# Performance work log

Hardware: AMD Instinct MI355X
Metric: run time of the kernel (lower is better)

## Reference

```python
import jax, jax.numpy as jnp
import numpy as np

B, S, D = 4, 2048, 512
H, DK = 16, 32  # n_heads, d_k == d_v == args.mid_dim


def setup_inputs() -> dict:
    key = jax.random.key(0)
    ks = jax.random.split(key, 9)
    s = 0.02
    return {
        "x": jax.random.normal(ks[0], (B, S, D), dtype=jnp.float32),
        "Wq": jax.random.normal(ks[1], (D, H * DK), dtype=jnp.float32) * s,
        "bq": jnp.zeros((H * DK,), dtype=jnp.float32),
        "Wk": jax.random.normal(ks[2], (D, H * DK), dtype=jnp.float32) * s,
        "bk": jnp.zeros((H * DK,), dtype=jnp.float32),
        "Wv": jax.random.normal(ks[3], (D, H * DK), dtype=jnp.float32) * s,
        "bv": jnp.zeros((H * DK,), dtype=jnp.float32),
        "Wo": jax.random.normal(ks[4], (H * DK, D), dtype=jnp.float32) * s,
        "bo": jnp.zeros((D,), dtype=jnp.float32),
        "mask_border": 64,
    }


def reference(x, Wq, bq, Wk, bk, Wv, bv, Wo, bo, mask_border):
    b, s, d = x.shape
    # band mask: tril(ones, border) * triu(ones, -border) == 1 where |i-j| <= border
    i = jnp.arange(s)
    band = (jnp.abs(i[:, None] - i[None, :]) <= mask_border).astype(x.dtype)  # [S,S]

    q = (x @ Wq + bq).reshape(b, s, H, DK)
    k = (x @ Wk + bk).reshape(b, s, H, DK)
    v = (x @ Wv + bv).reshape(b, s, H, DK)

    scale = 1.0 / jnp.sqrt(jnp.asarray(DK, x.dtype))
    # float attn_mask is ADDED to scores (PatchTST-style _ScaledDotProductAttention)
    scores = jnp.einsum("bihd,bjhd->bhij", q, k) * scale + band[None, None]
    attn = jax.nn.softmax(scores, axis=-1)
    o = jnp.einsum("bhij,bjhd->bihd", attn, v).reshape(b, s, H * DK)
    out_1 = o @ Wo + bo  # [B,S,D]

    # reconstruction score + quantiles (side stats; do not feed returned tensor)
    rec_score = jnp.mean((out_1 - x) ** 2, axis=2)  # [B,S]
    q1, q2, q3 = jnp.quantile(rec_score, jnp.array([0.25, 0.5, 0.75], rec_score.dtype), axis=-1)
    del q1, q2, q3

    # tmp = out_1 - x; out_1 = x + tmp  (identity); module returns out_1
    return out_1
```

## Files before the change

### kernel.cpp

```cpp
#include <hip/hip_runtime.h>
#include <hip/hip_bf16.h>

#define B_ 4
#define S_ 2048
#define D_ 512
#define H_ 16
#define DK_ 32
#define MS_ 8192

typedef unsigned short u16;
typedef __attribute__((ext_vector_type(4))) unsigned short u16x4;
typedef __attribute__((ext_vector_type(8))) short bf16x8;
typedef __attribute__((ext_vector_type(4))) float f32x4;

union pbu { unsigned u[4]; bf16x8 v; };

__device__ __forceinline__ u16 f2b(float f) {
    union { float f; unsigned u; } uf; uf.f = f;
    unsigned u = uf.u;
    unsigned r = u + 0x7fffu + ((u >> 16) & 1u);
    return (u16)(r >> 16);
}

__device__ __forceinline__ unsigned cvt_pk_bf16(float lo, float hi) {
    unsigned r;
    asm("v_cvt_pk_bf16_f32 %0, %1, %2" : "=v"(r) : "v"(lo), "v"(hi));
    return r;
}

__device__ __forceinline__ void gload16(const u16* src, u16* dst) {
    __builtin_amdgcn_global_load_lds(
        (const __attribute__((address_space(1))) unsigned int*)src,
        (__attribute__((address_space(3))) unsigned int*)dst, 16, 0, 0);
}

__global__ void cast_f32_to_bf16(const float* __restrict__ in, u16* __restrict__ out, int n4) {
    int i = blockIdx.x * blockDim.x + threadIdx.x;
    if (i >= n4) return;
    f32x4 v = *(const f32x4*)(in + (size_t)i * 4);
    u16x4 o;
    o[0] = f2b(v[0]); o[1] = f2b(v[1]); o[2] = f2b(v[2]); o[3] = f2b(v[3]);
    *(u16x4*)(out + (size_t)i * 4) = o;
}

__global__ void transpose_cast(const float* __restrict__ Wq, const float* __restrict__ Wk,
                               const float* __restrict__ Wv, const float* __restrict__ Wo,
                               u16* __restrict__ out) {
    const int z = blockIdx.z;
    const float* W = (z == 0) ? Wq : (z == 1) ? Wk : (z == 2) ? Wv : Wo;
    u16* O = out + (size_t)z * D_ * D_;
    __shared__ float T[32][33];
    const int n0 = blockIdx.x * 32, k0 = blockIdx.y * 32;
    const int tx = threadIdx.x & 31, ty = threadIdx.x >> 5;
#pragma unroll
    for (int i = 0; i < 4; i++) {
        int row = ty + 8 * i;
        T[tx][row] = W[(size_t)(k0 + row) * D_ + n0 + tx];
    }
    __syncthreads();
#pragma unroll
    for (int i = 0; i < 4; i++) {
        int row = ty + 8 * i;
        O[(size_t)(n0 + row) * D_ + k0 + tx] = f2b(T[row][tx]);
    }
}

__launch_bounds__(256)
__global__ void gemm_qkv(const u16* __restrict__ Xb, const u16* __restrict__ WT,
                         const float* __restrict__ bq, const float* __restrict__ bk, const float* __restrict__ bv,
                         u16* __restrict__ Qw, u16* __restrict__ Kw, u16* __restrict__ Vw) {
    const int which = blockIdx.z;
    const u16* Wt = WT + (size_t)which * D_ * D_;
    const float* bias = (which == 0) ? bq : (which == 1) ? bk : bv;
    u16* Out = (which == 0) ? Qw : (which == 1) ? Kw : Vw;
    const float oscale = (which == 0) ? (float)(1.4426950408889634 / 5.656854249492381) : 1.0f;

    __shared__ __attribute__((aligned(16))) u16 As[128][64];
    __shared__ __attribute__((aligned(16))) u16 Bs[128][64];

    const int tid = threadIdx.x;
    const int lane = tid & 63, w = tid >> 6;
    const int wr = w >> 1, wc = w & 1;
    const int g = lane >> 4, c = lane & 15;
    const int bm0 = blockIdx.y * 128, bn0 = blockIdx.x * 128;

    const int trow = tid >> 3;
    const int tcg = (tid & 7) ^ (trow & 7);
    const u16* gA = Xb + (size_t)(bm0 + trow) * D_ + 8 * tcg;
    const u16* gB = Wt + (size_t)(bn0 + trow) * D_ + 8 * tcg;

    f32x4 acc[4][4];
#pragma unroll
    for (int i = 0; i < 4; i++)
#pragma unroll
        for (int j = 0; j < 4; j++) acc[i][j] = (f32x4)0.0f;

    for (int k0 = 0; k0 < D_; k0 += 64) {
#pragma unroll
        for (int i = 0; i < 4; i++) {
            gload16(gA + (size_t)(32 * i) * D_ + k0, &As[0][0] + 512 * w + 2048 * i);
            gload16(gB + (size_t)(32 * i) * D_ + k0, &Bs[0][0] + 512 * w + 2048 * i);
        }
        __syncthreads();
#pragma unroll
        for (int kk = 0; kk < 2; kk++) {
            bf16x8 a[4], b[4];
#pragma unroll
            for (int mi = 0; mi < 4; mi++)
                a[mi] = *(const bf16x8*)&As[wr * 64 + 16 * mi + c][8 * ((4 * kk + g) ^ (c & 7))];
#pragma unroll
            for (int ni = 0; ni < 4; ni++)
                b[ni] = *(const bf16x8*)&Bs[wc * 64 + 16 * ni + c][8 * ((4 * kk + g) ^ (c & 7))];
#pragma unroll
            for (int mi = 0; mi < 4; mi++)
#pragma unroll
                for (int ni = 0; ni < 4; ni++)
                    acc[mi][ni] = __builtin_amdgcn_mfma_f32_16x16x32_bf16(a[mi], b[ni], acc[mi][ni], 0, 0, 0);
        }
        __syncthreads();
    }
#pragma unroll
    for (int mi = 0; mi < 4; mi++)
#pragma unroll
        for (int ni = 0; ni < 4; ni++)
#pragma unroll
            for (int r = 0; r < 4; r++) {
                int m = bm0 + wr * 64 + 16 * mi + 4 * g + r;
                int n = bn0 + wc * 64 + 16 * ni + c;
                float v = (acc[mi][ni][r] + bias[n]) * oscale;
                int b = m >> 11, s = m & 2047;
                int h = n >> 5, dk = n & 31;
                Out[(((size_t)(b * H_ + h) * S_) + s) * DK_ + dk] = f2b(v);
            }
}

__launch_bounds__(512)
__global__ void attn_kernel(const u16* __restrict__ Q, const u16* __restrict__ K,
                            const u16* __restrict__ V, u16* __restrict__ O,
                            const int* __restrict__ mbp) {
    const int border = *mbp;
    const unsigned b2u = (unsigned)(2 * border);
    const int bh = blockIdx.x;
    const int q0 = blockIdx.y * 256;
    const int tid = threadIdx.x;
    const int lane = tid & 63;
    const int w = __builtin_amdgcn_readfirstlane(tid >> 6);
    const int g = lane >> 4, c = lane & 15;

    __shared__ __attribute__((aligned(16))) u16 Ks[128][32];
    __shared__ __attribute__((aligned(16))) u16 Vt[2][32][68];

    const u16* Qbh = Q + (size_t)bh * S_ * DK_;
    const u16* Kbh = K + (size_t)bh * S_ * DK_;
    const u16* Vbh = V + (size_t)bh * S_ * DK_;

    const int qw0 = q0 + w * 32;
    const int qiA = qw0 + c;
    const int qiB = qw0 + 16 + c;
    const bf16x8 qfA = *(const bf16x8*)&Qbh[(size_t)qiA * DK_ + 8 * g];
    const bf16x8 qfB = *(const bf16x8*)&Qbh[(size_t)qiB * DK_ + 8 * g];

    f32x4 accO[2][2];
    f32x4 accL[2];
#pragma unroll
    for (int i = 0; i < 2; i++) { accO[i][0] = (f32x4)0.0f; accO[i][1] = (f32x4)0.0f; accL[i] = (f32x4)0.0f; }

    const float C2 = 1.4426950408889634f;

    union { u16x4 h[2]; bf16x8 v; } ones;
#pragma unroll
    for (int j = 0; j < 4; j++) { ones.h[0][j] = 0x3F80; ones.h[1][j] = 0x3F80; }

    const int gl_L = 16 * w + (lane >> 2);
    const int gl_gr = (gl_L & 64) + (gl_L & 3) + 4 * ((gl_L >> 5) & 1)
                    + 8 * ((gl_L >> 2) & 3) + 32 * ((gl_L >> 4) & 1);
    const u16* ksrc = Kbh + (size_t)gl_gr * DK_ + 8 * (lane & 3);
    u16* kdst = &Ks[0][0] + (w << 9);

    const int skk = tid >> 3;
    const int sc4 = (tid & 7) << 2;
    const u16* vp0 = Vbh + (size_t)skk * DK_ + sc4;

    auto sm_pack = [&](const f32x4* sf, int qs0, int qiv, int kvs, pbu* pb) {
        float e[4][4];
        const bool aOut = (qs0 > kvs + 63 + border) || (qs0 + 15 + border < kvs);
        const bool aIn  = (qs0 + 15 <= kvs + border) && (kvs + 63 <= qs0 + border);
        if (aOut) {
#pragma unroll
            for (int ct = 0; ct < 4; ct++)
#pragma unroll
                for (int r = 0; r < 4; r++)
                    e[ct][r] = __builtin_amdgcn_exp2f(sf[ct][r]);
        } else if (aIn) {
#pragma unroll
            for (int ct = 0; ct < 4; ct++)
#pragma unroll
                for (int r = 0; r < 4; r++)
                    e[ct][r] = __builtin_amdgcn_exp2f(sf[ct][r] + C2);
        } else {
            const int qb = qiv + border - kvs;
#pragma unroll
            for (int ct = 0; ct < 4; ct++) {
                const int k0l = 32 * (ct & 1) + 8 * g + 4 * (ct >> 1);
#pragma unroll
                for (int r = 0; r < 4; r++) {
                    float a = ((unsigned)(qb - (k0l + r)) <= b2u) ? C2 : 0.0f;
                    e[ct][r] = __builtin_amdgcn_exp2f(sf[ct][r] + a);
                }
            }
        }
        pb[0].u[0] = cvt_pk_bf16(e[0][0], e[0][1]);
        pb[0].u[1] = cvt_pk_bf16(e[0][2], e[0][3]);
        pb[0].u[2] = cvt_pk_bf16(e[2][0], e[2][1]);
        pb[0].u[3] = cvt_pk_bf16(e[2][2], e[2][3]);
        pb[1].u[0] = cvt_pk_bf16(e[1][0], e[1][1]);
        pb[1].u[1] = cvt_pk_bf16(e[1][2], e[1][3]);
        pb[1].u[2] = cvt_pk_bf16(e[3][0], e[3][1]);
        pb[1].u[3] = cvt_pk_bf16(e[3][2], e[3][3]);
    };

    auto do_sub = [&](int sub, int kvs) {
        f32x4 sA[4], sB[4];
#pragma unroll
        for (int ct = 0; ct < 4; ct++) {
            const bf16x8 kf = *(const bf16x8*)&Ks[sub * 64 + 16 * ct + c][8 * g];
            sA[ct] = __builtin_amdgcn_mfma_f32_16x16x32_bf16(kf, qfA, (f32x4)0.0f, 0, 0, 0);
            sB[ct] = __builtin_amdgcn_mfma_f32_16x16x32_bf16(kf, qfB, (f32x4)0.0f, 0, 0, 0);
        }
        pbu pA[2], pB[2];
        sm_pack(sA, qw0, qiA, kvs, pA);
        sm_pack(sB, qw0 + 16, qiB, kvs, pB);
#pragma unroll
        for (int t2 = 0; t2 < 2; t2++) {
#pragma unroll
            for (int ksl = 0; ksl < 2; ksl++) {
                union { u16x4 h[2]; bf16x8 v; } vf;
                vf.h[0] = *(const u16x4*)&Vt[sub][16 * t2 + c][32 * ksl + 8 * g];
                vf.h[1] = *(const u16x4*)&Vt[sub][16 * t2 + c][32 * ksl + 8 * g + 4];
                accO[0][t2] = __builtin_amdgcn_mfma_f32_16x16x32_bf16(vf.v, pA[ksl].v, accO[0][t2], 0, 0, 0);
                accO[1][t2] = __builtin_amdgcn_mfma_f32_16x16x32_bf16(vf.v, pB[ksl].v, accO[1][t2], 0, 0, 0);
            }
        }
#pragma unroll
        for (int ksl = 0; ksl < 2; ksl++) {
            accL[0] = __builtin_amdgcn_mfma_f32_16x16x32_bf16(ones.v, pA[ksl].v, accL[0], 0, 0, 0);
            accL[1] = __builtin_amdgcn_mfma_f32_16x16x32_bf16(ones.v, pB[ksl].v, accL[1], 0, 0, 0);
        }
    };

    u16x4 va = *(const u16x4*)vp0;
    u16x4 vb = *(const u16x4*)(vp0 + 64 * DK_);

    for (int kv0 = 0; kv0 < S_; kv0 += 128) {
        gload16(ksrc + (size_t)kv0 * DK_, kdst);
#pragma unroll
        for (int j = 0; j < 4; j++) {
            Vt[0][sc4 + j][skk] = va[j];
            Vt[1][sc4 + j][skk] = vb[j];
        }
        __syncthreads();

        if (kv0 + 128 < S_) {
            va = *(const u16x4*)(vp0 + (size_t)(kv0 + 128) * DK_);
            vb = *(const u16x4*)(vp0 + (size_t)(kv0 + 192) * DK_);
        }

        __builtin_amdgcn_s_setprio(1);
        do_sub(0, kv0);
        do_sub(1, kv0 + 64);
        __builtin_amdgcn_s_setprio(0);

        __syncthreads();
    }

    const int b = bh >> 4, h = bh & 15;
    const float linvA = 1.0f / accL[0][0];
    const float linvB = 1.0f / accL[1][0];
#pragma unroll
    for (int t2 = 0; t2 < 2; t2++) {
        u16x4 oA, oB;
#pragma unroll
        for (int r = 0; r < 4; r++) {
            oA[r] = f2b(accO[0][t2][r] * linvA);
            oB[r] = f2b(accO[1][t2][r] * linvB);
        }
        *(u16x4*)&O[((size_t)(b * S_ + qiA) * H_ + h) * DK_ + 16 * t2 + 4 * g] = oA;
        *(u16x4*)&O[((size_t)(b * S_ + qiB) * H_ + h) * DK_ + 16 * t2 + 4 * g] = oB;
    }
}

__launch_bounds__(256)
__global__ void gemm_out(const u16* __restrict__ Ob, const u16* __restrict__ WoT,
                         const float* __restrict__ bo, float* __restrict__ out) {
    __shared__ __attribute__((aligned(16))) u16 As[128][64];
    __shared__ __attribute__((aligned(16))) u16 Bs[128][64];

    const int tid = threadIdx.x;
    const int lane = tid & 63, w = tid >> 6;
    const int wr = w >> 1, wc = w & 1;
    const int g = lane >> 4, c = lane & 15;
    const int bm0 = blockIdx.y * 128, bn0 = blockIdx.x * 128;

    const int trow = tid >> 3;
    const int tcg = (tid & 7) ^ (trow & 7);
    const u16* gA = Ob + (size_t)(bm0 + trow) * D_ + 8 * tcg;
    const u16* gB = WoT + (size_t)(bn0 + trow) * D_ + 8 * tcg;

    f32x4 acc[4][4];
#pragma unroll
    for (int i = 0; i < 4; i++)
#pragma unroll
        for (int j = 0; j < 4; j++) acc[i][j] = (f32x4)0.0f;

    for (int k0 = 0; k0 < D_; k0 += 64) {
#pragma unroll
        for (int i = 0; i < 4; i++) {
            gload16(gA + (size_t)(32 * i) * D_ + k0, &As[0][0] + 512 * w + 2048 * i);
            gload16(gB + (size_t)(32 * i) * D_ + k0, &Bs[0][0] + 512 * w + 2048 * i);
        }
        __syncthreads();
#pragma unroll
        for (int kk = 0; kk < 2; kk++) {
            bf16x8 a[4], b[4];
#pragma unroll
            for (int mi = 0; mi < 4; mi++)
                a[mi] = *(const bf16x8*)&As[wr * 64 + 16 * mi + c][8 * ((4 * kk + g) ^ (c & 7))];
#pragma unroll
            for (int ni = 0; ni < 4; ni++)
                b[ni] = *(const bf16x8*)&Bs[wc * 64 + 16 * ni + c][8 * ((4 * kk + g) ^ (c & 7))];
#pragma unroll
            for (int mi = 0; mi < 4; mi++)
#pragma unroll
                for (int ni = 0; ni < 4; ni++)
                    acc[mi][ni] = __builtin_amdgcn_mfma_f32_16x16x32_bf16(a[mi], b[ni], acc[mi][ni], 0, 0, 0);
        }
        __syncthreads();
    }
#pragma unroll
    for (int mi = 0; mi < 4; mi++)
#pragma unroll
        for (int ni = 0; ni < 4; ni++)
#pragma unroll
            for (int r = 0; r < 4; r++) {
                int m = bm0 + wr * 64 + 16 * mi + 4 * g + r;
                int n = bn0 + wc * 64 + 16 * ni + c;
                out[(size_t)m * D_ + n] = acc[mi][ni][r] + bo[n];
            }
}

extern "C" void kernel_launch(void* const* d_in, const int* in_sizes, int n_in,
                              void* d_out, int out_size, void* d_ws, size_t ws_size,
                              hipStream_t stream) {
    const float* x  = (const float*)d_in[0];
    const float* Wq = (const float*)d_in[1];
    const float* bq = (const float*)d_in[2];
    const float* Wk = (const float*)d_in[3];
    const float* bk = (const float*)d_in[4];
    const float* Wv = (const float*)d_in[5];
    const float* bv = (const float*)d_in[6];
    const float* Wo = (const float*)d_in[7];
    const float* bo = (const float*)d_in[8];
    const int* mb   = (const int*)d_in[9];
    float* out = (float*)d_out;

    char* p = (char*)d_ws;
    u16* xb = (u16*)p; p += (size_t)MS_ * D_ * 2;
    u16* wt = (u16*)p; p += (size_t)4 * D_ * D_ * 2;
    u16* qw = (u16*)p; p += (size_t)MS_ * D_ * 2;
    u16* kw = (u16*)p; p += (size_t)MS_ * D_ * 2;
    u16* vw = (u16*)p; p += (size_t)MS_ * D_ * 2;
    u16* ow = (u16*)p; p += (size_t)MS_ * D_ * 2;

    cast_f32_to_bf16<<<4096, 256, 0, stream>>>(x, xb, MS_ * D_ / 4);
    transpose_cast<<<dim3(16, 16, 4), 256, 0, stream>>>(Wq, Wk, Wv, Wo, wt);

    gemm_qkv<<<dim3(4, 64, 3), 256, 0, stream>>>(xb, wt, bq, bk, bv, qw, kw, vw);
    attn_kernel<<<dim3(64, 8), 512, 0, stream>>>(qw, kw, vw, ow, mb);
    gemm_out<<<dim3(4, 64), 256, 0, stream>>>(ow, wt + (size_t)3 * D_ * D_, bo, out);
}
```

Measured before the change: 99.31 us.

## Double-buffer K tiles in attention and merge prep kernels into one launch

The attention kernel now keeps two K buffers in shared memory and issues the async global-to-LDS load for the next K tile before computing on the current one. This hides K load latency behind the MFMA work. Separately, the x cast and the weight transpose-cast are merged into a single prep kernel, saving one launch. The cost is extra LDS per block, which may lower occupancy, and the correctness of reusing a buffer now depends on the existing barriers.

```diff
diff --git a/kernel.cpp b/kernel.cpp
--- a/kernel.cpp
+++ b/kernel.cpp
@@ -34,34 +34,35 @@
         (__attribute__((address_space(3))) unsigned int*)dst, 16, 0, 0);
 }
 
-__global__ void cast_f32_to_bf16(const float* __restrict__ in, u16* __restrict__ out, int n4) {
-    int i = blockIdx.x * blockDim.x + threadIdx.x;
-    if (i >= n4) return;
-    f32x4 v = *(const f32x4*)(in + (size_t)i * 4);
-    u16x4 o;
-    o[0] = f2b(v[0]); o[1] = f2b(v[1]); o[2] = f2b(v[2]); o[3] = f2b(v[3]);
-    *(u16x4*)(out + (size_t)i * 4) = o;
-}
-
-__global__ void transpose_cast(const float* __restrict__ Wq, const float* __restrict__ Wk,
-                               const float* __restrict__ Wv, const float* __restrict__ Wo,
-                               u16* __restrict__ out) {
-    const int z = blockIdx.z;
-    const float* W = (z == 0) ? Wq : (z == 1) ? Wk : (z == 2) ? Wv : Wo;
-    u16* O = out + (size_t)z * D_ * D_;
-    __shared__ float T[32][33];
-    const int n0 = blockIdx.x * 32, k0 = blockIdx.y * 32;
-    const int tx = threadIdx.x & 31, ty = threadIdx.x >> 5;
-#pragma unroll
-    for (int i = 0; i < 4; i++) {
-        int row = ty + 8 * i;
-        T[tx][row] = W[(size_t)(k0 + row) * D_ + n0 + tx];
-    }
-    __syncthreads();
-#pragma unroll
-    for (int i = 0; i < 4; i++) {
-        int row = ty + 8 * i;
-        O[(size_t)(n0 + row) * D_ + k0 + tx] = f2b(T[row][tx]);
+__global__ void prep(const float* __restrict__ x,
+                     const float* __restrict__ Wq, const float* __restrict__ Wk,
+                     const float* __restrict__ Wv, const float* __restrict__ Wo,
+                     u16* __restrict__ xb, u16* __restrict__ wt) {
+    const int bid = blockIdx.x;
+    if (bid < 1024) {
+        const int z = bid >> 8, t = bid & 255;
+        const float* W = (z == 0) ? Wq : (z == 1) ? Wk : (z == 2) ? Wv : Wo;
+        u16* O = wt + (size_t)z * D_ * D_;
+        __shared__ float T[32][33];
+        const int n0 = (t & 15) * 32, k0 = (t >> 4) * 32;
+        const int tx = threadIdx.x & 31, ty = threadIdx.x >> 5;
+#pragma unroll
+        for (int i = 0; i < 4; i++) {
+            int row = ty + 8 * i;
+            T[tx][row] = W[(size_t)(k0 + row) * D_ + n0 + tx];
+        }
+        __syncthreads();
+#pragma unroll
+        for (int i = 0; i < 4; i++) {
+            int row = ty + 8 * i;
+            O[(size_t)(n0 + row) * D_ + k0 + tx] = f2b(T[row][tx]);
+        }
+    } else {
+        const int i = (bid - 1024) * 256 + threadIdx.x;
+        f32x4 v = *(const f32x4*)(x + (size_t)i * 4);
+        u16x4 o;
+        o[0] = f2b(v[0]); o[1] = f2b(v[1]); o[2] = f2b(v[2]); o[3] = f2b(v[3]);
+        *(u16x4*)(xb + (size_t)i * 4) = o;
     }
 }
 
@@ -147,7 +148,7 @@
     const int w = __builtin_amdgcn_readfirstlane(tid >> 6);
     const int g = lane >> 4, c = lane & 15;
 
-    __shared__ __attribute__((aligned(16))) u16 Ks[128][32];
+    __shared__ __attribute__((aligned(16))) u16 Ks[2][128][32];
     __shared__ __attribute__((aligned(16))) u16 Vt[2][32][68];
 
     const u16* Qbh = Q + (size_t)bh * S_ * DK_;
@@ -175,7 +176,8 @@
     const int gl_gr = (gl_L & 64) + (gl_L & 3) + 4 * ((gl_L >> 5) & 1)
                     + 8 * ((gl_L >> 2) & 3) + 32 * ((gl_L >> 4) & 1);
     const u16* ksrc = Kbh + (size_t)gl_gr * DK_ + 8 * (lane & 3);
-    u16* kdst = &Ks[0][0] + (w << 9);
+    u16* kb0 = &Ks[0][0][0] + (w << 9);
+    u16* kb1 = &Ks[1][0][0] + (w << 9);
 
     const int skk = tid >> 3;
     const int sc4 = (tid & 7) << 2;
@@ -219,11 +221,11 @@
         pb[1].u[3] = cvt_pk_bf16(e[3][2], e[3][3]);
     };
 
-    auto do_sub = [&](int sub, int kvs) {
+    auto do_sub = [&](const u16 (*Kb)[32], int sub, int kvs) {
         f32x4 sA[4], sB[4];
 #pragma unroll
         for (int ct = 0; ct < 4; ct++) {
-            const bf16x8 kf = *(const bf16x8*)&Ks[sub * 64 + 16 * ct + c][8 * g];
+            const bf16x8 kf = *(const bf16x8*)&Kb[sub * 64 + 16 * ct + c][8 * g];
             sA[ct] = __builtin_amdgcn_mfma_f32_16x16x32_bf16(kf, qfA, (f32x4)0.0f, 0, 0, 0);
             sB[ct] = __builtin_amdgcn_mfma_f32_16x16x32_bf16(kf, qfB, (f32x4)0.0f, 0, 0, 0);
         }
@@ -248,11 +250,12 @@
         }
     };
 
+    gload16(ksrc, kb0);
     u16x4 va = *(const u16x4*)vp0;
     u16x4 vb = *(const u16x4*)(vp0 + 64 * DK_);
 
+    int cur = 0;
     for (int kv0 = 0; kv0 < S_; kv0 += 128) {
-        gload16(ksrc + (size_t)kv0 * DK_, kdst);
 #pragma unroll
         for (int j = 0; j < 4; j++) {
             Vt[0][sc4 + j][skk] = va[j];
@@ -261,16 +264,19 @@
         __syncthreads();
 
         if (kv0 + 128 < S_) {
+            gload16(ksrc + (size_t)(kv0 + 128) * DK_, cur ? kb0 : kb1);
             va = *(const u16x4*)(vp0 + (size_t)(kv0 + 128) * DK_);
             vb = *(const u16x4*)(vp0 + (size_t)(kv0 + 192) * DK_);
         }
 
+        const u16 (*Kb)[32] = Ks[cur];
         __builtin_amdgcn_s_setprio(1);
-        do_sub(0, kv0);
-        do_sub(1, kv0 + 64);
+        do_sub(Kb, 0, kv0);
+        do_sub(Kb, 1, kv0 + 64);
         __builtin_amdgcn_s_setprio(0);
 
         __syncthreads();
+        cur ^= 1;
     }
 
     const int b = bh >> 4, h = bh & 15;
@@ -371,8 +377,7 @@
     u16* vw = (u16*)p; p += (size_t)MS_ * D_ * 2;
     u16* ow = (u16*)p; p += (size_t)MS_ * D_ * 2;
 
-    cast_f32_to_bf16<<<4096, 256, 0, stream>>>(x, xb, MS_ * D_ / 4);
-    transpose_cast<<<dim3(16, 16, 4), 256, 0, stream>>>(Wq, Wk, Wv, Wo, wt);
+    prep<<<5120, 256, 0, stream>>>(x, Wq, Wk, Wv, Wo, xb, wt);
 
     gemm_qkv<<<dim3(4, 64, 3), 256, 0, stream>>>(xb, wt, bq, bk, bv, qw, kw, vw);
     attn_kernel<<<dim3(64, 8), 512, 0, stream>>>(qw, kw, vw, ow, mb);
```

Measured after the change: 97.06 us. 1.02x faster.
